# Performance work log

Measured on AMD Instinct MI355X. Metric: run time of the kernel, lower is better.

The kernel has to match this reference:

```python
import jax, jax.numpy as jnp
import numpy as np

H = 200  # hidden size


def _init(k, shape):
    bound = 1.0 / np.sqrt(H)
    return jax.random.uniform(k, shape, jnp.float32, -bound, bound)


def setup_inputs() -> dict:
    key = jax.random.key(0)
    ks = jax.random.split(key, 11)
    T, B, D = 784, 512, 1
    x = jax.random.normal(ks[0], (T, 1, B, D), jnp.float32)
    return {
        "x": x,
        "W_in": _init(ks[1], (H, D)),
        "b_in": _init(ks[2], (H,)),
        # PyTorch LSTM gate order: i, f, g, o. b = b_ih + b_hh folded together.
        "Wih_f": _init(ks[3], (4 * H, H)),
        "Whh_f": _init(ks[4], (4 * H, H)),
        "b_f": _init(ks[5], (4 * H,)),
        "Wih_b": _init(ks[6], (4 * H, H)),
        "Whh_b": _init(ks[7], (4 * H, H)),
        "b_b": _init(ks[8], (4 * H,)),
        "W_fc": _init(ks[9], (10, 2 * H)),
        "b_fc": _init(ks[10], (10,)),
    }


def _lstm_dir(gates_in, Whh, reverse):
    # gates_in: (T, B, 4H) = x @ Wih.T + b, precomputed outside the scan.
    B = gates_in.shape[1]
    h0 = jnp.zeros((B, H), gates_in.dtype)

    def step(carry, g_in):
        h, c = carry
        g = g_in + h @ Whh.T  # (B, 4H)
        i, f, gg, o = jnp.split(g, 4, axis=-1)
        c = jax.nn.sigmoid(f) * c + jax.nn.sigmoid(i) * jnp.tanh(gg)
        h = jax.nn.sigmoid(o) * jnp.tanh(c)
        return (h, c), h

    _, hs = jax.lax.scan(step, (h0, h0), gates_in, reverse=reverse)
    return hs  # (T, B, H)


def reference(x, W_in, b_in, Wih_f, Whh_f, b_f, Wih_b, Whh_b, b_b, W_fc, b_fc):
    x = jnp.squeeze(x, 1)            # (T, B, D)
    x = x @ W_in.T + b_in            # (T, B, H)  input projection
    gf = x @ Wih_f.T + b_f           # (T, B, 4H) precomputed input gates, fwd dir
    gb = x @ Wih_b.T + b_b           # (T, B, 4H) precomputed input gates, bwd dir
    hf = _lstm_dir(gf, Whh_f, reverse=False)
    hb = _lstm_dir(gb, Whh_b, reverse=True)
    h = jnp.concatenate([hf, hb], axis=-1)  # (T, B, 2H)
    out = h @ W_fc.T + b_fc                 # (T, B, 10)
    return out.mean(axis=1)                 # (T, 10) -- matches x.mean(1)
```

## Files before the change

### kernel.cpp

```cpp
#include <hip/hip_runtime.h>


typedef short short8 __attribute__((ext_vector_type(8)));
typedef float f32x4 __attribute__((ext_vector_type(4)));
typedef unsigned short ushort_t;

#define T_STEPS 784
#define BATCH   512
#define HID     200
#define NKT     7
#define NMT     50
#define THREADS 512
#define HBUF    3584
#define NLDST   18
#define DYN_LDS (2 * HBUF * 2 + NLDST * NKT * 512 * 2)

#define HPART_FLOATS ((size_t)T_STEPS * 64 * 200)
#define WS_HPART 0
#define WS_UV    (40140800)
#define WS_WSW   (40140800 + 12800)

#define ACLOB \
  "a0","a1","a2","a3","a4","a5","a6","a7","a8","a9","a10","a11","a12","a13", \
  "a14","a15","a16","a17","a18","a19","a20","a21","a22","a23","a24","a25",   \
  "a26","a27","a28","a29","a30","a31","a32","a33","a34","a35","a36","a37",   \
  "a38","a39","a40","a41","a42","a43","a44","a45","a46","a47","a48","a49",   \
  "a50","a51","a52","a53","a54","a55","a56","a57","a58","a59","a60","a61",   \
  "a62","a63","a64","a65","a66","a67","a68","a69","a70","a71","a72","a73",   \
  "a74","a75","a76","a77","a78","a79","a80","a81","a82","a83","a84","a85",   \
  "a86","a87","a88","a89","a90","a91","a92","a93","a94","a95","a96","a97",   \
  "a98","a99","a100","a101","a102","a103","a104","a105","a106","a107",       \
  "a108","a109","a110","a111"

__device__ __forceinline__ ushort_t f2bf(float f) {
  union { float f; unsigned u; } x; x.f = f;
  return (ushort_t)((x.u + 0x7FFFu + ((x.u >> 16) & 1u)) >> 16);
}
__device__ __forceinline__ float bf2f(ushort_t u) {
  union { unsigned u; float f; } x; x.u = (unsigned)u << 16; return x.f;
}

__device__ __forceinline__ float row16_sum(float v) {
  union { float f; int i; } a, b;
  a.f = v;
  b.i = __builtin_amdgcn_update_dpp(0, a.i, 0x118, 0xF, 0xF, true); a.f += b.f;
  b.i = __builtin_amdgcn_update_dpp(0, a.i, 0x114, 0xF, 0xF, true); a.f += b.f;
  b.i = __builtin_amdgcn_update_dpp(0, a.i, 0x112, 0xF, 0xF, true); a.f += b.f;
  b.i = __builtin_amdgcn_update_dpp(0, a.i, 0x111, 0xF, 0xF, true); a.f += b.f;
  return a.f;
}

#define PIN1(T, K, N0, N1, N2, N3)                                            \
  {                                                                           \
    union { short8 s; unsigned u[4]; } cv;                                    \
    cv.s = *(const short8*)(wg +                                              \
        ((size_t)((rbase + (T)) * NKT + (K))) * 512 + lane * 8);              \
    asm volatile("v_accvgpr_write_b32 a" #N0 ", %0\n\t"                       \
                 "v_accvgpr_write_b32 a" #N1 ", %1\n\t"                       \
                 "v_accvgpr_write_b32 a" #N2 ", %2\n\t"                       \
                 "v_accvgpr_write_b32 a" #N3 ", %3"                           \
                 :: "v"(cv.u[0]), "v"(cv.u[1]), "v"(cv.u[2]), "v"(cv.u[3])    \
                 : "a" #N0, "a" #N1, "a" #N2, "a" #N3);                       \
  }

__global__ void prep_uv(const float* __restrict__ Wih_f, const float* __restrict__ b_f,
                        const float* __restrict__ Wih_b, const float* __restrict__ b_b,
                        const float* __restrict__ W_in, const float* __restrict__ b_in,
                        float* __restrict__ uv_g) {
  const int dir = blockIdx.x, j = threadIdx.x;
  if (j >= HID) return;
  const float* Wih = dir ? Wih_b : Wih_f;
  const float* b   = dir ? b_b   : b_f;
  for (int q = 0; q < 4; ++q) {
    const int row = q * HID + j;
    const float* wr = Wih + (size_t)row * HID;
    float u = 0.f, v = 0.f;
    for (int k = 0; k < HID; ++k) {
      u = fmaf(wr[k], W_in[k], u);
      v = fmaf(wr[k], b_in[k], v);
    }
    uv_g[(size_t)dir * 1600 + j * 8 + q]     = u;
    uv_g[(size_t)dir * 1600 + j * 8 + 4 + q] = v + b[row];
  }
}

__global__ void prep_w(const float* __restrict__ Whh_f, const float* __restrict__ Whh_b,
                       const float* __restrict__ uv_g, ushort_t* __restrict__ w_sw) {
  const int bid = blockIdx.x, lane = threadIdx.x;
  const int dir = bid / (NMT * NKT);
  const int rem = bid % (NMT * NKT);
  const int mt = rem / NKT, kt = rem % NKT;
  const float* W = dir ? Whh_b : Whh_f;
  const int m = lane & 15;
  const int q = m & 3;
  const int j = mt * 4 + (m >> 2);
  const int row = q * HID + j;
  const int grp = lane >> 4;
  short8 v8 = {0, 0, 0, 0, 0, 0, 0, 0};
  if (kt < 6) {
#pragma unroll
    for (int e = 0; e < 8; ++e)
      v8[e] = (short)f2bf(W[(size_t)row * HID + kt * 32 + grp * 8 + e]);
  } else if (grp == 0) {
#pragma unroll
    for (int e = 0; e < 8; ++e)
      v8[e] = (short)f2bf(W[(size_t)row * HID + 192 + e]);
  } else if (grp == 1) {
    const float U = uv_g[(size_t)dir * 1600 + j * 8 + q];
    const float V = uv_g[(size_t)dir * 1600 + j * 8 + 4 + q];
    const ushort_t vhi = f2bf(V), uhi = f2bf(U);
    v8[0] = (short)vhi;
    v8[1] = (short)f2bf(V - bf2f(vhi));
    v8[2] = (short)uhi;
    v8[3] = (short)f2bf(U - bf2f(uhi));
    v8[4] = (short)uhi;
  }
  *(short8*)(w_sw + (size_t)bid * 512 + (size_t)lane * 8) = v8;
}

__device__ __forceinline__ void cell_update(const f32x4 a, const int haddr,
                                            ushort_t* __restrict__ hnext,
                                            float& c, float& hold) {
  const float L1 = 1.44269504088896340736f;
  const float ei = __builtin_amdgcn_exp2f(fminf(-L1 * a[0], 30.f));
  const float ef = __builtin_amdgcn_exp2f(fminf(-L1 * a[1], 30.f));
  const float eg = __builtin_amdgcn_exp2f(fminf(-2.f * L1 * a[2], 30.f));
  const float eo = __builtin_amdgcn_exp2f(fminf(-L1 * a[3], 30.f));
  const float pi = 1.f + ei, pf = 1.f + ef, pg = 1.f + eg;
  const float pig = pi * pg;
  const float R1 = __builtin_amdgcn_rcpf(pig * pf);
  const float sf = pig * R1;
  const float sitg = (1.f - eg) * pf * R1;
  const float cn = fmaf(sf, c, sitg);
  c = cn;
  const float ec = __builtin_amdgcn_exp2f(fminf(-2.f * L1 * cn, 83.f));
  const float R2 = __builtin_amdgcn_rcpf((1.f + ec) * (1.f + eo));
  const float h = (1.f - ec) * R2;
  hnext[haddr] = f2bf(h);
  hold = row16_sum(h);
}

template <int NLDS>
__device__ __forceinline__ void scan_loop(
    const int rbase, const int lfirst, const int dir, const int b0,
    const int lane, const int wv, const int blk, const ushort_t* __restrict__ wg,
    const float* __restrict__ x, float* __restrict__ hpart,
    ushort_t* __restrict__ h_lds, const ushort_t* __restrict__ w_lds_my) {
  constexpr int NREG = 4;
  constexpr int NT = NREG + NLDS;
  const int bcol = lane & 15, krow = lane >> 4;
  const bool xw = (wv == 0) & (krow == 1);

  PIN1(0, 0,  0,  1,  2,  3)  PIN1(0, 1,  4,  5,  6,  7)
  PIN1(0, 2,  8,  9, 10, 11)  PIN1(0, 3, 12, 13, 14, 15)
  PIN1(0, 4, 16, 17, 18, 19)  PIN1(0, 5, 20, 21, 22, 23)
  PIN1(0, 6, 24, 25, 26, 27)
  PIN1(1, 0, 28, 29, 30, 31)  PIN1(1, 1, 32, 33, 34, 35)
  PIN1(1, 2, 36, 37, 38, 39)  PIN1(1, 3, 40, 41, 42, 43)
  PIN1(1, 4, 44, 45, 46, 47)  PIN1(1, 5, 48, 49, 50, 51)
  PIN1(1, 6, 52, 53, 54, 55)
  PIN1(2, 0, 56, 57, 58, 59)  PIN1(2, 1, 60, 61, 62, 63)
  PIN1(2, 2, 64, 65, 66, 67)  PIN1(2, 3, 68, 69, 70, 71)
  PIN1(2, 4, 72, 73, 74, 75)  PIN1(2, 5, 76, 77, 78, 79)
  PIN1(2, 6, 80, 81, 82, 83)
  PIN1(3, 0, 84, 85, 86, 87)  PIN1(3, 1, 88, 89, 90, 91)
  PIN1(3, 2, 92, 93, 94, 95)  PIN1(3, 3, 96, 97, 98, 99)
  PIN1(3, 4, 100, 101, 102, 103)  PIN1(3, 5, 104, 105, 106, 107)
  PIN1(3, 6, 108, 109, 110, 111)
  asm volatile("s_nop 7\n\ts_nop 7");

  f32x4 zero4 = {0.f, 0.f, 0.f, 0.f};
  asm volatile("" : "+v"(zero4));

  int haddr[NT];
#pragma unroll
  for (int i = 0; i < NT; ++i) {
    const int tile = (i < NREG) ? rbase + i : lfirst + (i - NREG);
    const int j = tile * 4 + krow;
    haddr[i] = (j >> 5) * 512 + (bcol | (((j >> 3) & 3) << 4)) * 8 + (j & 7);
  }
  float c[NT], hold[NT];
#pragma unroll
  for (int i = 0; i < NT; ++i) { c[i] = 0.f; hold[i] = 0.f; }

  const int jb = rbase * 4 + krow;
  const int jl = lfirst * 4 + krow;
  int t_prev = 0, cur = 0;

  for (int s = 0; s < T_STEPS; ++s) {
    const int t = dir ? (T_STEPS - 1 - s) : s;

    short8 bf[NKT];
#pragma unroll
    for (int kt = 0; kt < NKT; ++kt)
      bf[kt] = *(const short8*)&h_lds[cur * HBUF + kt * 512 + lane * 8];

    const int sn = (s + 1 < T_STEPS) ? s + 1 : s;
    float xn = 0.f;
    if (xw) xn = x[(size_t)(dir ? T_STEPS - 1 - sn : sn) * BATCH + b0 + bcol];

    if (s > 0 && bcol == 15) {
      float* hp = hpart + ((size_t)t_prev * 64 + blk) * 200;
#pragma unroll
      for (int i = 0; i < NREG; ++i) hp[jb + 4 * i] = hold[i];
#pragma unroll
      for (int i = 0; i < NLDS; ++i) hp[jl + 4 * i] = hold[NREG + i];
    }

    ushort_t* hnext = h_lds + (cur ^ 1) * HBUF;

    f32x4 a0, a1, a2, a3;
    asm volatile(
      "s_nop 1\n\t"
      "v_mfma_f32_16x16x32_bf16 %0, a[0:3],    %4, %11\n\t"
      "v_mfma_f32_16x16x32_bf16 %1, a[28:31],  %4, %11\n\t"
      "v_mfma_f32_16x16x32_bf16 %2, a[56:59],  %4, %11\n\t"
      "v_mfma_f32_16x16x32_bf16 %3, a[84:87],  %4, %11\n\t"
      "v_mfma_f32_16x16x32_bf16 %0, a[4:7],    %5, %0\n\t"
      "v_mfma_f32_16x16x32_bf16 %1, a[32:35],  %5, %1\n\t"
      "v_mfma_f32_16x16x32_bf16 %2, a[60:63],  %5, %2\n\t"
      "v_mfma_f32_16x16x32_bf16 %3, a[88:91],  %5, %3\n\t"
      "v_mfma_f32_16x16x32_bf16 %0, a[8:11],   %6, %0\n\t"
      "v_mfma_f32_16x16x32_bf16 %1, a[36:39],  %6, %1\n\t"
      "v_mfma_f32_16x16x32_bf16 %2, a[64:67],  %6, %2\n\t"
      "v_mfma_f32_16x16x32_bf16 %3, a[92:95],  %6, %3\n\t"
      "v_mfma_f32_16x16x32_bf16 %0, a[12:15],  %7, %0\n\t"
      "v_mfma_f32_16x16x32_bf16 %1, a[40:43],  %7, %1\n\t"
      "v_mfma_f32_16x16x32_bf16 %2, a[68:71],  %7, %2\n\t"
      "v_mfma_f32_16x16x32_bf16 %3, a[96:99],  %7, %3\n\t"
      "v_mfma_f32_16x16x32_bf16 %0, a[16:19],  %8, %0\n\t"
      "v_mfma_f32_16x16x32_bf16 %1, a[44:47],  %8, %1\n\t"
      "v_mfma_f32_16x16x32_bf16 %2, a[72:75],  %8, %2\n\t"
      "v_mfma_f32_16x16x32_bf16 %3, a[100:103],%8, %3\n\t"
      "v_mfma_f32_16x16x32_bf16 %0, a[20:23],  %9, %0\n\t"
      "v_mfma_f32_16x16x32_bf16 %1, a[48:51],  %9, %1\n\t"
      "v_mfma_f32_16x16x32_bf16 %2, a[76:79],  %9, %2\n\t"
      "v_mfma_f32_16x16x32_bf16 %3, a[104:107],%9, %3\n\t"
      "v_mfma_f32_16x16x32_bf16 %0, a[24:27],  %10, %0\n\t"
      "v_mfma_f32_16x16x32_bf16 %1, a[52:55],  %10, %1\n\t"
      "v_mfma_f32_16x16x32_bf16 %2, a[80:83],  %10, %2\n\t"
      "v_mfma_f32_16x16x32_bf16 %3, a[108:111],%10, %3\n\t"
      "s_nop 7\n\ts_nop 7"
      : "=&v"(a0), "=&v"(a1), "=&v"(a2), "=&v"(a3)
      : "v"(bf[0]), "v"(bf[1]), "v"(bf[2]), "v"(bf[3]), "v"(bf[4]),
        "v"(bf[5]), "v"(bf[6]), "v"(zero4)
      : ACLOB);
    cell_update(a0, haddr[0], hnext, c[0], hold[0]);
    cell_update(a1, haddr[1], hnext, c[1], hold[1]);
    cell_update(a2, haddr[2], hnext, c[2], hold[2]);
    cell_update(a3, haddr[3], hnext, c[3], hold[3]);

#pragma unroll
    for (int p = 0; p + 1 < NLDS; p += 2) {
      const int i0 = NREG + p, i1 = NREG + p + 1;
      f32x4 b0r, b1r;
      {
        const short8 af0 = *(const short8*)&w_lds_my[((p)     * NKT + 0) * 512 + lane * 8];
        const short8 af1 = *(const short8*)&w_lds_my[((p + 1) * NKT + 0) * 512 + lane * 8];
        asm volatile("s_nop 1\n\t"
                     "v_mfma_f32_16x16x32_bf16 %0, %2, %4, %5\n\t"
                     "v_mfma_f32_16x16x32_bf16 %1, %3, %4, %5"
                     : "=&v"(b0r), "=&v"(b1r)
                     : "v"(af0), "v"(af1), "v"(bf[0]), "v"(zero4));
      }
#pragma unroll
      for (int kt = 1; kt < NKT - 1; ++kt) {
        const short8 af0 = *(const short8*)&w_lds_my[((p)     * NKT + kt) * 512 + lane * 8];
        const short8 af1 = *(const short8*)&w_lds_my[((p + 1) * NKT + kt) * 512 + lane * 8];
        asm volatile("v_mfma_f32_16x16x32_bf16 %0, %2, %4, %0\n\t"
                     "v_mfma_f32_16x16x32_bf16 %1, %3, %4, %1"
                     : "+v"(b0r), "+v"(b1r)
                     : "v"(af0), "v"(af1), "v"(bf[kt]));
      }
      {
        const short8 af0 = *(const short8*)&w_lds_my[((p)     * NKT + 6) * 512 + lane * 8];
        const short8 af1 = *(const short8*)&w_lds_my[((p + 1) * NKT + 6) * 512 + lane * 8];
        asm volatile("v_mfma_f32_16x16x32_bf16 %0, %2, %4, %0\n\t"
                     "v_mfma_f32_16x16x32_bf16 %1, %3, %4, %1\n\t"
                     "s_nop 7\n\ts_nop 7"
                     : "+v"(b0r), "+v"(b1r)
                     : "v"(af0), "v"(af1), "v"(bf[6]));
      }
      cell_update(b0r, haddr[i0], hnext, c[i0], hold[i0]);
      cell_update(b1r, haddr[i1], hnext, c[i1], hold[i1]);
    }
    if constexpr (NLDS & 1) {
      constexpr int p = NLDS - 1;
      const int i0 = NREG + p;
      f32x4 b0r;
      {
        const short8 af = *(const short8*)&w_lds_my[(p * NKT + 0) * 512 + lane * 8];
        asm volatile("s_nop 1\n\t"
                     "v_mfma_f32_16x16x32_bf16 %0, %1, %2, %3"
                     : "=&v"(b0r) : "v"(af), "v"(bf[0]), "v"(zero4));
      }
#pragma unroll
      for (int kt = 1; kt < NKT - 1; ++kt) {
        const short8 af = *(const short8*)&w_lds_my[(p * NKT + kt) * 512 + lane * 8];
        asm volatile("v_mfma_f32_16x16x32_bf16 %0, %1, %2, %0"
                     : "+v"(b0r) : "v"(af), "v"(bf[kt]));
      }
      {
        const short8 af = *(const short8*)&w_lds_my[(p * NKT + 6) * 512 + lane * 8];
        asm volatile("v_mfma_f32_16x16x32_bf16 %0, %1, %2, %0\n\t"
                     "s_nop 7\n\ts_nop 7"
                     : "+v"(b0r) : "v"(af), "v"(bf[6]));
      }
      cell_update(b0r, haddr[i0], hnext, c[i0], hold[i0]);
    }

    if (xw) {
      const ushort_t hi = f2bf(xn);
      const ushort_t lo = f2bf(xn - bf2f(hi));
      const int sb = 6 * 512 + lane * 8;
      hnext[sb + 2] = hi;
      hnext[sb + 3] = hi;
      hnext[sb + 4] = lo;
    }

    t_prev = t;
    asm volatile("s_waitcnt lgkmcnt(0)\n\ts_barrier" ::: "memory");
    cur ^= 1;
  }
  if (bcol == 15) {
    float* hp = hpart + ((size_t)t_prev * 64 + blk) * 200;
#pragma unroll
    for (int i = 0; i < NREG; ++i) hp[jb + 4 * i] = hold[i];
#pragma unroll
    for (int i = 0; i < NLDS; ++i) hp[jl + 4 * i] = hold[NREG + i];
  }
}

__global__ __launch_bounds__(THREADS, 2) void lstm_main(
    const float* __restrict__ x, const ushort_t* __restrict__ w_sw,
    float* __restrict__ hpart) {
  extern __shared__ __align__(16) ushort_t dynlds[];
  ushort_t* h_lds = dynlds;
  ushort_t* w_lds = dynlds + 2 * HBUF;

  const int tid = threadIdx.x;
  const int lane = tid & 63;
  const int wv = tid >> 6;
  const int blk = blockIdx.x;
  const int dir = blk & 1;
  const int b0 = (blk >> 1) * 16;

  const ushort_t* wg = w_sw + (size_t)dir * NMT * NKT * 512;

  for (int i = tid; i < HBUF; i += THREADS) ((unsigned*)h_lds)[i] = 0;
  for (int i = tid; i < NLDST * NKT * 64; i += THREADS)
    *(short8*)&w_lds[(size_t)i * 8] =
        *(const short8*)(wg + (size_t)32 * NKT * 512 + (size_t)i * 8);
  __syncthreads();

  if (tid < 16) {
    const int t0 = dir ? T_STEPS - 1 : 0;
    const float x0 = x[(size_t)t0 * BATCH + b0 + tid];
    const ushort_t hi = f2bf(x0);
    const ushort_t lo = f2bf(x0 - bf2f(hi));
    const int sb = 6 * 512 + (16 + tid) * 8;
    h_lds[sb + 0] = 0x3F80; h_lds[sb + 1] = 0x3F80;
    h_lds[HBUF + sb + 0] = 0x3F80; h_lds[HBUF + sb + 1] = 0x3F80;
    h_lds[sb + 2] = hi; h_lds[sb + 3] = hi; h_lds[sb + 4] = lo;
  }
  __syncthreads();

  const int rbase = 4 * wv;
  const int lfirst = (wv < 6) ? (32 + 2 * wv) : (44 + 3 * (wv - 6));
  const ushort_t* wl = w_lds + (size_t)(lfirst - 32) * NKT * 512;
  if (wv < 6)
    scan_loop<2>(rbase, lfirst, dir, b0, lane, wv, blk, wg, x, hpart, h_lds, wl);
  else
    scan_loop<3>(rbase, lfirst, dir, b0, lane, wv, blk, wg, x, hpart, h_lds, wl);
}

__global__ void out_proj(const float* __restrict__ hpart, const float* __restrict__ Wfc,
                         const float* __restrict__ bfc, float* __restrict__ out) {
  const int t = blockIdx.x, tid = threadIdx.x;
  const float* hb = hpart + (size_t)t * 64 * 200;
  float a[10] = {0.f, 0.f, 0.f, 0.f, 0.f, 0.f, 0.f, 0.f, 0.f, 0.f};
  for (int col = tid; col < 400; col += 256) {
    const int dir = (col >= HID) ? 1 : 0;
    const int j = col - dir * HID;
    float s = 0.f;
#pragma unroll
    for (int sl = 0; sl < 32; ++sl) s += hb[(size_t)((sl << 1) | dir) * 200 + j];
    const float hv = s * (1.f / 512.f);
#pragma unroll
    for (int o = 0; o < 10; ++o) a[o] = fmaf(hv, Wfc[o * 400 + col], a[o]);
  }
#pragma unroll
  for (int o = 0; o < 10; ++o) {
    float v = a[o];
    for (int m = 32; m; m >>= 1) v += __shfl_xor(v, m);
    a[o] = v;
  }
  __shared__ float red[4][10];
  if ((tid & 63) == 0)
#pragma unroll
    for (int o = 0; o < 10; ++o) red[tid >> 6][o] = a[o];
  __syncthreads();
  if (tid < 10)
    out[t * 10 + tid] = bfc[tid] + red[0][tid] + red[1][tid] + red[2][tid] + red[3][tid];
}

extern "C" void kernel_launch(void* const* d_in, const int* in_sizes, int n_in,
                              void* d_out, int out_size, void* d_ws, size_t ws_size,
                              hipStream_t stream) {
  const float* x     = (const float*)d_in[0];
  const float* W_in  = (const float*)d_in[1];
  const float* b_in  = (const float*)d_in[2];
  const float* Wih_f = (const float*)d_in[3];
  const float* Whh_f = (const float*)d_in[4];
  const float* b_f   = (const float*)d_in[5];
  const float* Wih_b = (const float*)d_in[6];
  const float* Whh_b = (const float*)d_in[7];
  const float* b_b   = (const float*)d_in[8];
  const float* W_fc  = (const float*)d_in[9];
  const float* b_fc  = (const float*)d_in[10];
  float* out = (float*)d_out;

  char* ws = (char*)d_ws;
  float*    hpart = (float*)(ws + WS_HPART);
  float*    uv_g  = (float*)(ws + WS_UV);
  ushort_t* w_sw  = (ushort_t*)(ws + WS_WSW);

  hipFuncSetAttribute((const void*)lstm_main,
                      hipFuncAttributeMaxDynamicSharedMemorySize, DYN_LDS);

  prep_uv<<<2, 256, 0, stream>>>(Wih_f, b_f, Wih_b, b_b, W_in, b_in, uv_g);
  prep_w<<<2 * NMT * NKT, 64, 0, stream>>>(Whh_f, Whh_b, uv_g, w_sw);
  lstm_main<<<64, THREADS, DYN_LDS, stream>>>(x, w_sw, hpart);
  out_proj<<<T_STEPS, 256, 0, stream>>>(hpart, W_fc, b_fc, out);
}
```

Baseline: 1.636 ms.

## Pin five weight tiles per wave in AGPRs and store h partials immediately

Each wave now keeps five recurrent-weight M-tiles resident in accumulation registers instead of four, which shrinks the LDS-resident weight tiles from 18 to 10 and redistributes them as one or two per wave. The MFMA chain is split into a 3-tile group and a 2-tile group so cell updates for the first group can start sooner. Per-step partial h sums are written to global memory directly inside the cell update instead of being held in registers and written one step later. The goal is fewer LDS weight reads on the per-step critical path, at the cost of more AGPR pressure and global stores interleaved with the recurrence.

Result: slower. 1.769 ms (+8.1%).

```diff
diff --git a/kernel.cpp b/kernel.cpp
--- a/kernel.cpp
+++ b/kernel.cpp
@@ -12,10 +12,9 @@
 #define NMT     50
 #define THREADS 512
 #define HBUF    3584
-#define NLDST   18
+#define NLDST   10
 #define DYN_LDS (2 * HBUF * 2 + NLDST * NKT * 512 * 2)
 
-#define HPART_FLOATS ((size_t)T_STEPS * 64 * 200)
 #define WS_HPART 0
 #define WS_UV    (40140800)
 #define WS_WSW   (40140800 + 12800)
@@ -30,7 +29,10 @@
   "a74","a75","a76","a77","a78","a79","a80","a81","a82","a83","a84","a85",   \
   "a86","a87","a88","a89","a90","a91","a92","a93","a94","a95","a96","a97",   \
   "a98","a99","a100","a101","a102","a103","a104","a105","a106","a107",       \
-  "a108","a109","a110","a111"
+  "a108","a109","a110","a111","a112","a113","a114","a115","a116","a117",     \
+  "a118","a119","a120","a121","a122","a123","a124","a125","a126","a127",     \
+  "a128","a129","a130","a131","a132","a133","a134","a135","a136","a137",     \
+  "a138","a139"
 
 __device__ __forceinline__ ushort_t f2bf(float f) {
   union { float f; unsigned u; } x; x.f = f;
@@ -120,7 +122,8 @@
 
 __device__ __forceinline__ void cell_update(const f32x4 a, const int haddr,
                                             ushort_t* __restrict__ hnext,
-                                            float& c, float& hold) {
+                                            float& c, const bool st,
+                                            float* __restrict__ dst) {
   const float L1 = 1.44269504088896340736f;
   const float ei = __builtin_amdgcn_exp2f(fminf(-L1 * a[0], 30.f));
   const float ef = __builtin_amdgcn_exp2f(fminf(-L1 * a[1], 30.f));
@@ -137,58 +140,64 @@
   const float R2 = __builtin_amdgcn_rcpf((1.f + ec) * (1.f + eo));
   const float h = (1.f - ec) * R2;
   hnext[haddr] = f2bf(h);
-  hold = row16_sum(h);
+  const float vs = row16_sum(h);
+  if (st) *dst = vs;
 }
 
 template <int NLDS>
 __device__ __forceinline__ void scan_loop(
-    const int rbase, const int lfirst, const int dir, const int b0,
+    const int rbase, const int ltile, const int dir, const int b0,
     const int lane, const int wv, const int blk, const ushort_t* __restrict__ wg,
     const float* __restrict__ x, float* __restrict__ hpart,
     ushort_t* __restrict__ h_lds, const ushort_t* __restrict__ w_lds_my) {
-  constexpr int NREG = 4;
+  constexpr int NREG = 5;
   constexpr int NT = NREG + NLDS;
   const int bcol = lane & 15, krow = lane >> 4;
   const bool xw = (wv == 0) & (krow == 1);
-
-  PIN1(0, 0,  0,  1,  2,  3)  PIN1(0, 1,  4,  5,  6,  7)
-  PIN1(0, 2,  8,  9, 10, 11)  PIN1(0, 3, 12, 13, 14, 15)
-  PIN1(0, 4, 16, 17, 18, 19)  PIN1(0, 5, 20, 21, 22, 23)
-  PIN1(0, 6, 24, 25, 26, 27)
-  PIN1(1, 0, 28, 29, 30, 31)  PIN1(1, 1, 32, 33, 34, 35)
-  PIN1(1, 2, 36, 37, 38, 39)  PIN1(1, 3, 40, 41, 42, 43)
-  PIN1(1, 4, 44, 45, 46, 47)  PIN1(1, 5, 48, 49, 50, 51)
-  PIN1(1, 6, 52, 53, 54, 55)
-  PIN1(2, 0, 56, 57, 58, 59)  PIN1(2, 1, 60, 61, 62, 63)
-  PIN1(2, 2, 64, 65, 66, 67)  PIN1(2, 3, 68, 69, 70, 71)
-  PIN1(2, 4, 72, 73, 74, 75)  PIN1(2, 5, 76, 77, 78, 79)
-  PIN1(2, 6, 80, 81, 82, 83)
-  PIN1(3, 0, 84, 85, 86, 87)  PIN1(3, 1, 88, 89, 90, 91)
-  PIN1(3, 2, 92, 93, 94, 95)  PIN1(3, 3, 96, 97, 98, 99)
+  const bool st = (bcol == 15);
+
+  PIN1(0, 0,   0,   1,   2,   3)  PIN1(0, 1,   4,   5,   6,   7)
+  PIN1(0, 2,   8,   9,  10,  11)  PIN1(0, 3,  12,  13,  14,  15)
+  PIN1(0, 4,  16,  17,  18,  19)  PIN1(0, 5,  20,  21,  22,  23)
+  PIN1(0, 6,  24,  25,  26,  27)
+  PIN1(1, 0,  28,  29,  30,  31)  PIN1(1, 1,  32,  33,  34,  35)
+  PIN1(1, 2,  36,  37,  38,  39)  PIN1(1, 3,  40,  41,  42,  43)
+  PIN1(1, 4,  44,  45,  46,  47)  PIN1(1, 5,  48,  49,  50,  51)
+  PIN1(1, 6,  52,  53,  54,  55)
+  PIN1(2, 0,  56,  57,  58,  59)  PIN1(2, 1,  60,  61,  62,  63)
+  PIN1(2, 2,  64,  65,  66,  67)  PIN1(2, 3,  68,  69,  70,  71)
+  PIN1(2, 4,  72,  73,  74,  75)  PIN1(2, 5,  76,  77,  78,  79)
+  PIN1(2, 6,  80,  81,  82,  83)
+  PIN1(3, 0,  84,  85,  86,  87)  PIN1(3, 1,  88,  89,  90,  91)
+  PIN1(3, 2,  92,  93,  94,  95)  PIN1(3, 3,  96,  97,  98,  99)
   PIN1(3, 4, 100, 101, 102, 103)  PIN1(3, 5, 104, 105, 106, 107)
   PIN1(3, 6, 108, 109, 110, 111)
+  PIN1(4, 0, 112, 113, 114, 115)  PIN1(4, 1, 116, 117, 118, 119)
+  PIN1(4, 2, 120, 121, 122, 123)  PIN1(4, 3, 124, 125, 126, 127)
+  PIN1(4, 4, 128, 129, 130, 131)  PIN1(4, 5, 132, 133, 134, 135)
+  PIN1(4, 6, 136, 137, 138, 139)
   asm volatile("s_nop 7\n\ts_nop 7");
 
   f32x4 zero4 = {0.f, 0.f, 0.f, 0.f};
   asm volatile("" : "+v"(zero4));
 
-  int haddr[NT];
+  int haddr[NT], jidx[NT];
 #pragma unroll
   for (int i = 0; i < NT; ++i) {
-    const int tile = (i < NREG) ? rbase + i : lfirst + (i - NREG);
+    const int tile = (i < NREG) ? rbase + i : ltile + (i - NREG);
     const int j = tile * 4 + krow;
+    jidx[i] = j;
     haddr[i] = (j >> 5) * 512 + (bcol | (((j >> 3) & 3) << 4)) * 8 + (j & 7);
   }
-  float c[NT], hold[NT];
-#pragma unroll
-  for (int i = 0; i < NT; ++i) { c[i] = 0.f; hold[i] = 0.f; }
-
-  const int jb = rbase * 4 + krow;
-  const int jl = lfirst * 4 + krow;
-  int t_prev = 0, cur = 0;
+  float c[NT];
+#pragma unroll
+  for (int i = 0; i < NT; ++i) c[i] = 0.f;
+
+  int cur = 0;
 
   for (int s = 0; s < T_STEPS; ++s) {
     const int t = dir ? (T_STEPS - 1 - s) : s;
+    float* hp = hpart + ((size_t)t * 64 + blk) * 200;
 
     short8 bf[NKT];
 #pragma unroll
@@ -199,64 +208,92 @@
     float xn = 0.f;
     if (xw) xn = x[(size_t)(dir ? T_STEPS - 1 - sn : sn) * BATCH + b0 + bcol];
 
-    if (s > 0 && bcol == 15) {
-      float* hp = hpart + ((size_t)t_prev * 64 + blk) * 200;
-#pragma unroll
-      for (int i = 0; i < NREG; ++i) hp[jb + 4 * i] = hold[i];
-#pragma unroll
-      for (int i = 0; i < NLDS; ++i) hp[jl + 4 * i] = hold[NREG + i];
-    }
-
     ushort_t* hnext = h_lds + (cur ^ 1) * HBUF;
 
-    f32x4 a0, a1, a2, a3;
+    f32x4 a0, a1, a2;
     asm volatile(
       "s_nop 1\n\t"
-      "v_mfma_f32_16x16x32_bf16 %0, a[0:3],    %4, %11\n\t"
-      "v_mfma_f32_16x16x32_bf16 %1, a[28:31],  %4, %11\n\t"
-      "v_mfma_f32_16x16x32_bf16 %2, a[56:59],  %4, %11\n\t"
-      "v_mfma_f32_16x16x32_bf16 %3, a[84:87],  %4, %11\n\t"
-      "v_mfma_f32_16x16x32_bf16 %0, a[4:7],    %5, %0\n\t"
-      "v_mfma_f32_16x16x32_bf16 %1, a[32:35],  %5, %1\n\t"
-      "v_mfma_f32_16x16x32_bf16 %2, a[60:63],  %5, %2\n\t"
-      "v_mfma_f32_16x16x32_bf16 %3, a[88:91],  %5, %3\n\t"
-      "v_mfma_f32_16x16x32_bf16 %0, a[8:11],   %6, %0\n\t"
-      "v_mfma_f32_16x16x32_bf16 %1, a[36:39],  %6, %1\n\t"
-      "v_mfma_f32_16x16x32_bf16 %2, a[64:67],  %6, %2\n\t"
-      "v_mfma_f32_16x16x32_bf16 %3, a[92:95],  %6, %3\n\t"
-      "v_mfma_f32_16x16x32_bf16 %0, a[12:15],  %7, %0\n\t"
-      "v_mfma_f32_16x16x32_bf16 %1, a[40:43],  %7, %1\n\t"
-      "v_mfma_f32_16x16x32_bf16 %2, a[68:71],  %7, %2\n\t"
-      "v_mfma_f32_16x16x32_bf16 %3, a[96:99],  %7, %3\n\t"
-      "v_mfma_f32_16x16x32_bf16 %0, a[16:19],  %8, %0\n\t"
-      "v_mfma_f32_16x16x32_bf16 %1, a[44:47],  %8, %1\n\t"
-      "v_mfma_f32_16x16x32_bf16 %2, a[72:75],  %8, %2\n\t"
-      "v_mfma_f32_16x16x32_bf16 %3, a[100:103],%8, %3\n\t"
-      "v_mfma_f32_16x16x32_bf16 %0, a[20:23],  %9, %0\n\t"
-      "v_mfma_f32_16x16x32_bf16 %1, a[48:51],  %9, %1\n\t"
-      "v_mfma_f32_16x16x32_bf16 %2, a[76:79],  %9, %2\n\t"
-      "v_mfma_f32_16x16x32_bf16 %3, a[104:107],%9, %3\n\t"
-      "v_mfma_f32_16x16x32_bf16 %0, a[24:27],  %10, %0\n\t"
-      "v_mfma_f32_16x16x32_bf16 %1, a[52:55],  %10, %1\n\t"
-      "v_mfma_f32_16x16x32_bf16 %2, a[80:83],  %10, %2\n\t"
-      "v_mfma_f32_16x16x32_bf16 %3, a[108:111],%10, %3\n\t"
+      "v_mfma_f32_16x16x32_bf16 %0, a[0:3],    %3, %10\n\t"
+      "v_mfma_f32_16x16x32_bf16 %1, a[28:31],  %3, %10\n\t"
+      "v_mfma_f32_16x16x32_bf16 %2, a[56:59],  %3, %10\n\t"
+      "v_mfma_f32_16x16x32_bf16 %0, a[4:7],    %4, %0\n\t"
+      "v_mfma_f32_16x16x32_bf16 %1, a[32:35],  %4, %1\n\t"
+      "v_mfma_f32_16x16x32_bf16 %2, a[60:63],  %4, %2\n\t"
+      "v_mfma_f32_16x16x32_bf16 %0, a[8:11],   %5, %0\n\t"
+      "v_mfma_f32_16x16x32_bf16 %1, a[36:39],  %5, %1\n\t"
+      "v_mfma_f32_16x16x32_bf16 %2, a[64:67],  %5, %2\n\t"
+      "v_mfma_f32_16x16x32_bf16 %0, a[12:15],  %6, %0\n\t"
+      "v_mfma_f32_16x16x32_bf16 %1, a[40:43],  %6, %1\n\t"
+      "v_mfma_f32_16x16x32_bf16 %2, a[68:71],  %6, %2\n\t"
+      "v_mfma_f32_16x16x32_bf16 %0, a[16:19],  %7, %0\n\t"
+      "v_mfma_f32_16x16x32_bf16 %1, a[44:47],  %7, %1\n\t"
+      "v_mfma_f32_16x16x32_bf16 %2, a[72:75],  %7, %2\n\t"
+      "v_mfma_f32_16x16x32_bf16 %0, a[20:23],  %8, %0\n\t"
+      "v_mfma_f32_16x16x32_bf16 %1, a[48:51],  %8, %1\n\t"
+      "v_mfma_f32_16x16x32_bf16 %2, a[76:79],  %8, %2\n\t"
+      "v_mfma_f32_16x16x32_bf16 %0, a[24:27],  %9, %0\n\t"
+      "v_mfma_f32_16x16x32_bf16 %1, a[52:55],  %9, %1\n\t"
+      "v_mfma_f32_16x16x32_bf16 %2, a[80:83],  %9, %2\n\t"
       "s_nop 7\n\ts_nop 7"
-      : "=&v"(a0), "=&v"(a1), "=&v"(a2), "=&v"(a3)
+      : "=&v"(a0), "=&v"(a1), "=&v"(a2)
       : "v"(bf[0]), "v"(bf[1]), "v"(bf[2]), "v"(bf[3]), "v"(bf[4]),
         "v"(bf[5]), "v"(bf[6]), "v"(zero4)
       : ACLOB);
-    cell_update(a0, haddr[0], hnext, c[0], hold[0]);
-    cell_update(a1, haddr[1], hnext, c[1], hold[1]);
-    cell_update(a2, haddr[2], hnext, c[2], hold[2]);
-    cell_update(a3, haddr[3], hnext, c[3], hold[3]);
-
-#pragma unroll
-    for (int p = 0; p + 1 < NLDS; p += 2) {
-      const int i0 = NREG + p, i1 = NREG + p + 1;
+    cell_update(a0, haddr[0], hnext, c[0], st, hp + jidx[0]);
+    cell_update(a1, haddr[1], hnext, c[1], st, hp + jidx[1]);
+    cell_update(a2, haddr[2], hnext, c[2], st, hp + jidx[2]);
+
+    f32x4 a3, a4;
+    asm volatile(
+      "s_nop 1\n\t"
+      "v_mfma_f32_16x16x32_bf16 %0, a[84:87],   %2, %9\n\t"
+      "v_mfma_f32_16x16x32_bf16 %1, a[112:115], %2, %9\n\t"
+      "v_mfma_f32_16x16x32_bf16 %0, a[88:91],   %3, %0\n\t"
+      "v_mfma_f32_16x16x32_bf16 %1, a[116:119], %3, %1\n\t"
+      "v_mfma_f32_16x16x32_bf16 %0, a[92:95],   %4, %0\n\t"
+      "v_mfma_f32_16x16x32_bf16 %1, a[120:123], %4, %1\n\t"
+      "v_mfma_f32_16x16x32_bf16 %0, a[96:99],   %5, %0\n\t"
+      "v_mfma_f32_16x16x32_bf16 %1, a[124:127], %5, %1\n\t"
+      "v_mfma_f32_16x16x32_bf16 %0, a[100:103], %6, %0\n\t"
+      "v_mfma_f32_16x16x32_bf16 %1, a[128:131], %6, %1\n\t"
+      "v_mfma_f32_16x16x32_bf16 %0, a[104:107], %7, %0\n\t"
+      "v_mfma_f32_16x16x32_bf16 %1, a[132:135], %7, %1\n\t"
+      "v_mfma_f32_16x16x32_bf16 %0, a[108:111], %8, %0\n\t"
+      "v_mfma_f32_16x16x32_bf16 %1, a[136:139], %8, %1\n\t"
+      "s_nop 7\n\ts_nop 7"
+      : "=&v"(a3), "=&v"(a4)
+      : "v"(bf[0]), "v"(bf[1]), "v"(bf[2]), "v"(bf[3]), "v"(bf[4]),
+        "v"(bf[5]), "v"(bf[6]), "v"(zero4)
+      : ACLOB);
+    cell_update(a3, haddr[3], hnext, c[3], st, hp + jidx[3]);
+    cell_update(a4, haddr[4], hnext, c[4], st, hp + jidx[4]);
+
+    if constexpr (NLDS == 1) {
+      f32x4 b0r;
+      {
+        const short8 af = *(const short8*)&w_lds_my[0 * 512 + lane * 8];
+        asm volatile("s_nop 1\n\t"
+                     "v_mfma_f32_16x16x32_bf16 %0, %1, %2, %3"
+                     : "=&v"(b0r) : "v"(af), "v"(bf[0]), "v"(zero4));
+      }
+#pragma unroll
+      for (int kt = 1; kt < NKT - 1; ++kt) {
+        const short8 af = *(const short8*)&w_lds_my[kt * 512 + lane * 8];
+        asm volatile("v_mfma_f32_16x16x32_bf16 %0, %1, %2, %0"
+                     : "+v"(b0r) : "v"(af), "v"(bf[kt]));
+      }
+      {
+        const short8 af = *(const short8*)&w_lds_my[6 * 512 + lane * 8];
+        asm volatile("v_mfma_f32_16x16x32_bf16 %0, %1, %2, %0\n\t"
+                     "s_nop 7\n\ts_nop 7"
+                     : "+v"(b0r) : "v"(af), "v"(bf[6]));
+      }
+      cell_update(b0r, haddr[5], hnext, c[5], st, hp + jidx[5]);
+    } else {
       f32x4 b0r, b1r;
       {
-        const short8 af0 = *(const short8*)&w_lds_my[((p)     * NKT + 0) * 512 + lane * 8];
-        const short8 af1 = *(const short8*)&w_lds_my[((p + 1) * NKT + 0) * 512 + lane * 8];
+        const short8 af0 = *(const short8*)&w_lds_my[(0 * NKT + 0) * 512 + lane * 8];
+        const short8 af1 = *(const short8*)&w_lds_my[(1 * NKT + 0) * 512 + lane * 8];
         asm volatile("s_nop 1\n\t"
                      "v_mfma_f32_16x16x32_bf16 %0, %2, %4, %5\n\t"
                      "v_mfma_f32_16x16x32_bf16 %1, %3, %4, %5"
@@ -265,48 +302,24 @@
       }
 #pragma unroll
       for (int kt = 1; kt < NKT - 1; ++kt) {
-        const short8 af0 = *(const short8*)&w_lds_my[((p)     * NKT + kt) * 512 + lane * 8];
-        const short8 af1 = *(const short8*)&w_lds_my[((p + 1) * NKT + kt) * 512 + lane * 8];
+        const short8 af0 = *(const short8*)&w_lds_my[(0 * NKT + kt) * 512 + lane * 8];
+        const short8 af1 = *(const short8*)&w_lds_my[(1 * NKT + kt) * 512 + lane * 8];
         asm volatile("v_mfma_f32_16x16x32_bf16 %0, %2, %4, %0\n\t"
                      "v_mfma_f32_16x16x32_bf16 %1, %3, %4, %1"
                      : "+v"(b0r), "+v"(b1r)
                      : "v"(af0), "v"(af1), "v"(bf[kt]));
       }
       {
-        const short8 af0 = *(const short8*)&w_lds_my[((p)     * NKT + 6) * 512 + lane * 8];
-        const short8 af1 = *(const short8*)&w_lds_my[((p + 1) * NKT + 6) * 512 + lane * 8];
+        const short8 af0 = *(const short8*)&w_lds_my[(0 * NKT + 6) * 512 + lane * 8];
+        const short8 af1 = *(const short8*)&w_lds_my[(1 * NKT + 6) * 512 + lane * 8];
         asm volatile("v_mfma_f32_16x16x32_bf16 %0, %2, %4, %0\n\t"
                      "v_mfma_f32_16x16x32_bf16 %1, %3, %4, %1\n\t"
                      "s_nop 7\n\ts_nop 7"
                      : "+v"(b0r), "+v"(b1r)
                      : "v"(af0), "v"(af1), "v"(bf[6]));
       }
-      cell_update(b0r, haddr[i0], hnext, c[i0], hold[i0]);
-      cell_update(b1r, haddr[i1], hnext, c[i1], hold[i1]);
-    }
-    if constexpr (NLDS & 1) {
-      constexpr int p = NLDS - 1;
-      const int i0 = NREG + p;
-      f32x4 b0r;
-      {
-        const short8 af = *(const short8*)&w_lds_my[(p * NKT + 0) * 512 + lane * 8];
-        asm volatile("s_nop 1\n\t"
-                     "v_mfma_f32_16x16x32_bf16 %0, %1, %2, %3"
-                     : "=&v"(b0r) : "v"(af), "v"(bf[0]), "v"(zero4));
-      }
-#pragma unroll
-      for (int kt = 1; kt < NKT - 1; ++kt) {
-        const short8 af = *(const short8*)&w_lds_my[(p * NKT + kt) * 512 + lane * 8];
-        asm volatile("v_mfma_f32_16x16x32_bf16 %0, %1, %2, %0"
-                     : "+v"(b0r) : "v"(af), "v"(bf[kt]));
-      }
-      {
-        const short8 af = *(const short8*)&w_lds_my[(p * NKT + 6) * 512 + lane * 8];
-        asm volatile("v_mfma_f32_16x16x32_bf16 %0, %1, %2, %0\n\t"
-                     "s_nop 7\n\ts_nop 7"
-                     : "+v"(b0r) : "v"(af), "v"(bf[6]));
-      }
-      cell_update(b0r, haddr[i0], hnext, c[i0], hold[i0]);
+      cell_update(b0r, haddr[5], hnext, c[5], st, hp + jidx[5]);
+      cell_update(b1r, haddr[6], hnext, c[6], st, hp + jidx[6]);
     }
 
     if (xw) {
@@ -318,16 +331,8 @@
       hnext[sb + 4] = lo;
     }
 
-    t_prev = t;
     asm volatile("s_waitcnt lgkmcnt(0)\n\ts_barrier" ::: "memory");
     cur ^= 1;
-  }
-  if (bcol == 15) {
-    float* hp = hpart + ((size_t)t_prev * 64 + blk) * 200;
-#pragma unroll
-    for (int i = 0; i < NREG; ++i) hp[jb + 4 * i] = hold[i];
-#pragma unroll
-    for (int i = 0; i < NLDS; ++i) hp[jl + 4 * i] = hold[NREG + i];
   }
 }
 
@@ -350,7 +355,7 @@
   for (int i = tid; i < HBUF; i += THREADS) ((unsigned*)h_lds)[i] = 0;
   for (int i = tid; i < NLDST * NKT * 64; i += THREADS)
     *(short8*)&w_lds[(size_t)i * 8] =
-        *(const short8*)(wg + (size_t)32 * NKT * 512 + (size_t)i * 8);
+        *(const short8*)(wg + (size_t)40 * NKT * 512 + (size_t)i * 8);
   __syncthreads();
 
   if (tid < 16) {
@@ -365,13 +370,17 @@
   }
   __syncthreads();
 
-  const int rbase = 4 * wv;
-  const int lfirst = (wv < 6) ? (32 + 2 * wv) : (44 + 3 * (wv - 6));
-  const ushort_t* wl = w_lds + (size_t)(lfirst - 32) * NKT * 512;
-  if (wv < 6)
-    scan_loop<2>(rbase, lfirst, dir, b0, lane, wv, blk, wg, x, hpart, h_lds, wl);
-  else
-    scan_loop<3>(rbase, lfirst, dir, b0, lane, wv, blk, wg, x, hpart, h_lds, wl);
+  const int rbase = 5 * wv;
+  if (wv < 6) {
+    scan_loop<1>(rbase, 40 + wv, dir, b0, lane, wv, blk, wg, x, hpart, h_lds,
+                 w_lds + (size_t)wv * NKT * 512);
+  } else if (wv == 6) {
+    scan_loop<2>(rbase, 46, dir, b0, lane, wv, blk, wg, x, hpart, h_lds,
+                 w_lds + (size_t)6 * NKT * 512);
+  } else {
+    scan_loop<2>(rbase, 48, dir, b0, lane, wv, blk, wg, x, hpart, h_lds,
+                 w_lds + (size_t)8 * NKT * 512);
+  }
 }
 
 __global__ void out_proj(const float* __restrict__ hpart, const float* __restrict__ Wfc,
```
